# Optimization experiments

Hardware: AMD Instinct MI355X
Metric: run time of the kernel (lower is better)

The kernel has to match this reference:

```python
import jax, jax.numpy as jnp
import numpy as np

N = 10000      # nodes
E = 80000      # edges (avg degree 8)
G = 64         # graphs in batch
HID = 256
RBF_K = 16
DEPTH = 6
KA, KC, KE = 16, 6, 5
DE = HID // 3          # 85, per-modality embedding dim
CAT = 3 * HID + RBF_K  # 784, width of [h_i, h_j, rbf, e_emb]
CUTOFF = 10.0


def _gumbel_hard(probs, noise, tau=1.0):
    """F.gumbel_softmax(log(probs), tau, hard=True) with externally supplied gumbel noise."""
    logits = jnp.log(jnp.clip(probs, 1e-12))
    y = jax.nn.softmax((logits + noise) / tau, axis=-1)
    hard = jax.nn.one_hot(jnp.argmax(y, axis=-1), y.shape[-1], dtype=y.dtype)
    return hard + y - jax.lax.stop_gradient(y)  # straight-through


def setup_inputs() -> dict:
    key = jax.random.key(0)
    ks = iter(jax.random.split(key, 80))

    def nrm(shape, fan):
        return jax.random.normal(next(ks), shape, jnp.float32) / np.sqrt(fan).astype(np.float32)

    def gumbel(shape):
        u = jax.random.uniform(next(ks), shape, minval=1e-9, maxval=1.0 - 1e-9)
        return -jnp.log(-jnp.log(u))

    inp = {}
    inp['a_t'] = jax.random.uniform(next(ks), (N, KA))
    inp['c_t'] = jax.random.uniform(next(ks), (N, KC))
    inp['e_t'] = jax.random.uniform(next(ks), (E, KE))
    inp['x_t'] = jax.random.normal(next(ks), (N, 3))
    inp['g_a'] = gumbel((N, KA))
    inp['g_c'] = gumbel((N, KC))
    inp['g_e'] = gumbel((E, KE))

    # embeddings / fuse / lift
    inp['atom_W'] = nrm((KA, DE), KA)
    inp['charge_W'] = nrm((KC, DE), KC)
    inp['bond_W'] = nrm((KE, DE), KE)
    inp['fuse_W'] = nrm((3 * DE, HID), 3 * DE)
    inp['fuse_b'] = jnp.zeros((HID,))
    inp['lift_W'] = nrm((DE, HID), DE)
    inp['lift_b'] = jnp.zeros((HID,))

    # stacked block params (DEPTH blocks)
    inp['phim_W1'] = nrm((DEPTH, CAT, HID), CAT)
    inp['phim_b1'] = jnp.zeros((DEPTH, HID))
    inp['phim_W2'] = nrm((DEPTH, HID, HID), HID)
    inp['phim_b2'] = jnp.zeros((DEPTH, HID))
    inp['phix_W1'] = nrm((DEPTH, HID, HID), HID)
    inp['phix_b1'] = jnp.zeros((DEPTH, HID))
    inp['phix_W2'] = nrm((DEPTH, HID, 1), HID)
    inp['phix_b2'] = jnp.zeros((DEPTH, 1))
    inp['psim_W1'] = nrm((DEPTH, CAT, HID), CAT)
    inp['psim_b1'] = jnp.zeros((DEPTH, HID))
    inp['psim_W2'] = nrm((DEPTH, HID, HID), HID)
    inp['psim_b2'] = jnp.zeros((DEPTH, HID))
    inp['updh_W1'] = nrm((DEPTH, 2 * HID, HID), 2 * HID)
    inp['updh_b1'] = jnp.zeros((DEPTH, HID))
    inp['updh_W2'] = nrm((DEPTH, HID, HID), HID)
    inp['updh_b2'] = jnp.zeros((DEPTH, HID))
    inp['ln_g'] = jnp.ones((DEPTH, HID))
    inp['ln_b'] = jnp.zeros((DEPTH, HID))
    inp['head_W'] = nrm((HID, 1), HID)
    inp['head_b'] = jnp.zeros((1,))

    inp['src'] = jax.random.randint(next(ks), (E,), 0, N)
    inp['dst'] = jax.random.randint(next(ks), (E,), 0, N)
    inp['node_graph'] = jnp.sort(jax.random.randint(next(ks), (N,), 0, G))
    return inp


def reference(a_t, c_t, e_t, x_t, g_a, g_c, g_e,
              atom_W, charge_W, bond_W, fuse_W, fuse_b, lift_W, lift_b,
              phim_W1, phim_b1, phim_W2, phim_b2,
              phix_W1, phix_b1, phix_W2, phix_b2,
              psim_W1, psim_b1, psim_W2, psim_b2,
              updh_W1, updh_b1, updh_W2, updh_b2,
              ln_g, ln_b, head_W, head_b,
              src, dst, node_graph):
    centers = jnp.linspace(0.0, CUTOFF, RBF_K)
    widths = jnp.full((RBF_K,), CUTOFF / RBF_K)

    # encode nodes: gumbel-hard embed atom & charge probs, zero x-slot, fuse
    a_h = _gumbel_hard(a_t, g_a) @ atom_W           # (N, DE)
    c_h = _gumbel_hard(c_t, g_c) @ charge_W         # (N, DE)
    h = jnp.concatenate([a_h, c_h, jnp.zeros_like(a_h)], axis=-1) @ fuse_W + fuse_b  # (N, HID)
    # encode edges
    e_emb = (_gumbel_hard(e_t, g_e) @ bond_W) @ lift_W + lift_b  # (E, HID)

    x = x_t
    for d in range(DEPTH):
        h_i, h_j = h[dst], h[src]                    # gather per edge
        rij = x[dst] - x[src]                        # (E, 3)
        dist = jnp.sqrt(jnp.clip(jnp.sum(rij * rij, -1, keepdims=True), 0.0))
        z = (dist - centers) / (widths + 1e-12)
        rbf = jnp.exp(-0.5 * z * z)                  # (E, RBF_K)
        cat = jnp.concatenate([h_i, h_j, rbf, e_emb], axis=-1)  # (E, 784)
        m = jax.nn.silu(jax.nn.silu(cat @ phim_W1[d] + phim_b1[d]) @ phim_W2[d] + phim_b2[d])
        gate = jax.nn.silu(m @ phix_W1[d] + phix_b1[d]) @ phix_W2[d] + phix_b2[d]  # (E, 1)
        pm = jax.nn.silu(jax.nn.silu(cat @ psim_W1[d] + psim_b1[d]) @ psim_W2[d] + psim_b2[d])
        dx_sum = jax.ops.segment_sum(rij * gate, dst, num_segments=N)   # scatter to dst
        pm_sum = jax.ops.segment_sum(pm, dst, num_segments=N)
        x = x + dx_sum
        u = jax.nn.silu(jnp.concatenate([h, pm_sum], -1) @ updh_W1[d] + updh_b1[d]) @ updh_W2[d] + updh_b2[d]
        z2 = h + u
        mu = jnp.mean(z2, -1, keepdims=True)
        var = jnp.mean((z2 - mu) ** 2, -1, keepdims=True)
        h = (z2 - mu) / jnp.sqrt(var + 1e-5) * ln_g[d] + ln_b[d]

    # mean readout per graph
    cnt = jax.ops.segment_sum(jnp.ones((h.shape[0], 1), h.dtype), node_graph, num_segments=G)
    hg = jax.ops.segment_sum(h, node_graph, num_segments=G) / jnp.maximum(cnt, 1.0)
    out = jax.nn.sigmoid((hg @ head_W + head_b) / 2.0)  # property='score' -> sigmoid, tau=2
    return out
```

## Files before the change

kernel.cpp:

```cpp
#include <hip/hip_runtime.h>
#include <math.h>

#define NN   10000
#define NE   80000
#define NG   64
#define HID  256
#define RBFK 16
#define NDEP 6
#define KA   16
#define KC   6
#define KE   5
#define DE   85
#define CATW 784

typedef __attribute__((ext_vector_type(8))) short bf16x8;
typedef __attribute__((ext_vector_type(4))) float f32x4;
typedef __attribute__((ext_vector_type(2))) __bf16 bf16v2;

#if __has_builtin(__builtin_amdgcn_fdot2_f32_bf16)
#define HAVE_BF16_DOT2 1
#else
#define HAVE_BF16_DOT2 0
#endif

static __device__ __forceinline__ float silu_f(float v) {
  return __fdividef(v, 1.0f + __expf(-v));
}

static __device__ __forceinline__ unsigned short f2bf(float f) {
  union { float f; unsigned int u; } v; v.f = f;
  unsigned int r = v.u + 0x7fff + ((v.u >> 16) & 1);
  return (unsigned short)(r >> 16);
}
static __device__ __forceinline__ float bf2f(unsigned short h) {
  union { unsigned int u; float f; } v; v.u = ((unsigned int)h) << 16;
  return v.f;
}
static __device__ __forceinline__ bf16v2 u2bf2(unsigned int u) {
  union { unsigned int u; bf16v2 v; } x; x.u = u; return x.v;
}

static __device__ __forceinline__ void gload16(const void* g, void* l) {
  __builtin_amdgcn_global_load_lds((const __attribute__((address_space(1))) unsigned int*)g,
                                   (__attribute__((address_space(3))) unsigned int*)l, 16, 0, 0);
}

__global__ void convw_plain(const float* __restrict__ W, unsigned short* __restrict__ Wt, int K,
                            long long wt_dstride, int wt_rowoff) {
  __shared__ float T[32][65];
  int k0 = blockIdx.x * 32, n0 = blockIdx.y * 64, d = blockIdx.z;
  int tid = threadIdx.x;
  int nn = tid & 63, kr = tid >> 6;
  const float* Wd = W + (size_t)d * K * 256;
#pragma unroll
  for (int i = 0; i < 8; ++i) {
    int k = kr + i * 4;
    T[k][nn] = Wd[(size_t)(k0 + k) * 256 + n0 + nn];
  }
  __syncthreads();
  unsigned short* Wtd = Wt + (size_t)d * wt_dstride;
  int kk = tid & 31, nr = tid >> 5;
#pragma unroll
  for (int i = 0; i < 8; ++i) {
    int n = nr + i * 8;
    Wtd[(size_t)(wt_rowoff + n0 + n) * K + k0 + kk] = f2bf(T[kk][n]);
  }
}

__global__ void convw_nodeblk(const float* __restrict__ W, unsigned short* __restrict__ Wt,
                              int src_k0, int nt_base) {
  __shared__ float T[32][65];
  int k0 = blockIdx.x * 32, n0 = blockIdx.y * 64, d = blockIdx.z;
  int tid = threadIdx.x;
  int nn = tid & 63, kr = tid >> 6;
  const float* Wd = W + (size_t)d * CATW * 256;
#pragma unroll
  for (int i = 0; i < 8; ++i) {
    int k = kr + i * 4;
    T[k][nn] = Wd[(size_t)(src_k0 + k0 + k) * 256 + n0 + nn];
  }
  __syncthreads();
  unsigned short* Wtd = Wt + (size_t)d * 1024 * 256;
  int kk = tid & 31, nr = tid >> 5;
#pragma unroll
  for (int i = 0; i < 8; ++i) {
    int n = nr + i * 8;
    Wtd[(size_t)(nt_base + n0 + n) * 256 + k0 + kk] = f2bf(T[kk][n]);
  }
}

__global__ void convw_rbf(const float* __restrict__ phimW1, const float* __restrict__ psimW1,
                          unsigned short* __restrict__ wR) {
  int d = blockIdx.x, j = threadIdx.x;
  int jj = j & 255;
  const float* W = (j < 256) ? phimW1 : psimW1;
  for (int k = 0; k < 16; ++k)
    wR[((size_t)d * 16 + k) * 512 + j] = f2bf(W[(size_t)d * CATW * 256 + (size_t)(512 + k) * 256 + jj]);
}

__global__ void convw_rbf2(const float* __restrict__ phimW1, const float* __restrict__ psimW1,
                           unsigned int* __restrict__ wRp) {
  int d = blockIdx.x, j = threadIdx.x;
  int jj = j & 255;
  const float* W = (j < 256) ? phimW1 : psimW1;
  const float* base = W + (size_t)d * CATW * 256;
  for (int p = 0; p < 8; ++p) {
    unsigned int lo = f2bf(base[(size_t)(512 + 2*p) * 256 + jj]);
    unsigned int hi = f2bf(base[(size_t)(512 + 2*p + 1) * 256 + jj]);
    wRp[((size_t)d * 8 + p) * 512 + j] = lo | (hi << 16);
  }
}

__global__ void tables_kernel(const float* __restrict__ atom_W, const float* __restrict__ charge_W,
                              const float* __restrict__ bond_W, const float* __restrict__ fuse_W,
                              const float* __restrict__ fuse_b, const float* __restrict__ lift_W,
                              const float* __restrict__ lift_b,
                              float* __restrict__ tabA, float* __restrict__ tabC,
                              float* __restrict__ tabEf) {
  int r = blockIdx.x, k = threadIdx.x;
  if (r < KA) {
    float s = 0.f;
    for (int d = 0; d < DE; ++d) s += atom_W[r*DE + d] * fuse_W[d*HID + k];
    tabA[r*HID + k] = s + fuse_b[k];
  } else if (r < KA + KC) {
    int rr = r - KA;
    float s = 0.f;
    for (int d = 0; d < DE; ++d) s += charge_W[rr*DE + d] * fuse_W[(DE + d)*HID + k];
    tabC[rr*HID + k] = s;
  } else {
    int rr = r - KA - KC;
    float s = 0.f;
    for (int d = 0; d < DE; ++d) s += bond_W[rr*DE + d] * lift_W[d*HID + k];
    tabEf[rr*HID + k] = s + lift_b[k];
  }
}

__global__ void tabe1_kernel(const float* __restrict__ tabEf,
                             const float* __restrict__ phimW1, const float* __restrict__ phimb1,
                             const float* __restrict__ psimW1, const float* __restrict__ psimb1,
                             unsigned short* __restrict__ tabE1) {
  int r = blockIdx.x, d = blockIdx.y, j = threadIdx.x;
  const float* W = (j < 256) ? phimW1 : psimW1;
  const float* b = (j < 256) ? phimb1 : psimb1;
  int jj = j & 255;
  float s = b[d*256 + jj];
  for (int k = 0; k < 256; ++k)
    s += tabEf[r*256 + k] * W[(size_t)d*CATW*256 + (size_t)(528 + k)*256 + jj];
  tabE1[((size_t)d*5 + r)*512 + j] = f2bf(s);
}

__global__ void node_init_kernel(const float* __restrict__ a_t, const float* __restrict__ c_t,
                                 const float* __restrict__ g_a, const float* __restrict__ g_c,
                                 const float* __restrict__ x_t, const float* __restrict__ tabA,
                                 const float* __restrict__ tabC, float* __restrict__ h,
                                 unsigned short* __restrict__ hbf, float* __restrict__ x) {
  int n = blockIdx.x;
  __shared__ int s_ia, s_ic;
  if (threadIdx.x == 0) {
    float best = -1e30f; int bi = 0;
    for (int j = 0; j < KA; ++j) {
      float v = logf(fmaxf(a_t[n*KA + j], 1e-12f)) + g_a[n*KA + j];
      if (v > best) { best = v; bi = j; }
    }
    s_ia = bi;
  }
  if (threadIdx.x == 1) {
    float best = -1e30f; int bi = 0;
    for (int j = 0; j < KC; ++j) {
      float v = logf(fmaxf(c_t[n*KC + j], 1e-12f)) + g_c[n*KC + j];
      if (v > best) { best = v; bi = j; }
    }
    s_ic = bi;
  }
  __syncthreads();
  int k = threadIdx.x;
  float v = tabA[s_ia*HID + k] + tabC[s_ic*HID + k];
  h[n*HID + k] = v;
  hbf[n*HID + k] = f2bf(v);
  if (k < 3) x[n*3 + k] = x_t[n*3 + k];
}

__global__ void edge_init_kernel(const float* __restrict__ e_t, const float* __restrict__ g_e,
                                 int* __restrict__ ie) {
  int e = blockIdx.x * blockDim.x + threadIdx.x;
  if (e >= NE) return;
  float best = -1e30f; int bi = 0;
  for (int j = 0; j < KE; ++j) {
    float v = logf(fmaxf(e_t[e*KE + j], 1e-12f)) + g_e[e*KE + j];
    if (v > best) { best = v; bi = j; }
  }
  ie[e] = bi;
}

__global__ void hist_kernel(const int* __restrict__ dst, int* __restrict__ deg) {
  int e = blockIdx.x * 256 + threadIdx.x;
  if (e < NE) atomicAdd(&deg[dst[e]], 1);
}

__global__ void scan_kernel(const int* __restrict__ deg, int* __restrict__ rowstart,
                            int* __restrict__ cursor) {
  __shared__ int tmp[1024];
  int t = threadIdx.x;
  int base = t * 10;
  int local[10];
  int s = 0;
#pragma unroll
  for (int i = 0; i < 10; ++i) { local[i] = deg[base + i]; s += local[i]; }
  tmp[t] = s;
  __syncthreads();
  for (int off = 1; off < 1024; off <<= 1) {
    int v = (t >= off) ? tmp[t - off] : 0;
    __syncthreads();
    tmp[t] += v;
    __syncthreads();
  }
  int run = (t == 0) ? 0 : tmp[t - 1];
#pragma unroll
  for (int i = 0; i < 10; ++i) {
    rowstart[base + i] = run; cursor[base + i] = run; run += local[i];
  }
  if (t == 1023) rowstart[10240] = run;
}

__global__ void fill_kernel(const int* __restrict__ dst, int* __restrict__ cursor,
                            int* __restrict__ eids) {
  int e = blockIdx.x * 256 + threadIdx.x;
  if (e >= NE) return;
  int pos = atomicAdd(&cursor[dst[e]], 1);
  eids[pos] = e;
}

__global__ void sortrows_kernel(const int* __restrict__ rowstart, int* __restrict__ eids) {
  int n = blockIdx.x * 256 + threadIdx.x;
  if (n >= NN) return;
  int s = rowstart[n], e = rowstart[n + 1];
  for (int i = s + 1; i < e; ++i) {
    int v = eids[i]; int j = i - 1;
    while (j >= s && eids[j] > v) { eids[j + 1] = eids[j]; --j; }
    eids[j + 1] = v;
  }
}

__global__ void gbound_kernel(const int* __restrict__ ng, int* __restrict__ gstart) {
  int n = blockIdx.x * 256 + threadIdx.x;
  if (n >= NN) return;
  if (n == 0) {
    for (int g = 0; g <= ng[0]; ++g) gstart[g] = 0;
  } else {
    int a = ng[n-1], b = ng[n];
    for (int g = a + 1; g <= b; ++g) gstart[g] = n;
  }
  if (n == NN - 1) {
    for (int g = ng[n] + 1; g <= NG; ++g) gstart[g] = NN;
  }
}

__global__ __launch_bounds__(256) void combine2_kernel(
    const int* __restrict__ srcp, const int* __restrict__ dstp, const int* __restrict__ iep,
    const float* __restrict__ x,
    const unsigned short* __restrict__ P,
    const unsigned short* __restrict__ tabE1,
    const unsigned short* __restrict__ wR,
    const unsigned int* __restrict__ wRp,
    unsigned short* __restrict__ c1, unsigned short* __restrict__ ps1) {
  const int tid = threadIdx.x;
  const int lane = tid & 63;
  const int e = blockIdx.x * 4 + (tid >> 6);
  const int half = lane >> 5;
  const int c8 = (lane & 31) * 8;
  const int ds = dstp[e], sr = srcp[e], ib = iep[e];
  float r0 = x[ds*3+0] - x[sr*3+0];
  float r1 = x[ds*3+1] - x[sr*3+1];
  float r2 = x[ds*3+2] - x[sr*3+2];
  float dist = sqrtf(r0*r0 + r1*r1 + r2*r2);
  int klo = (int)(dist * 1.5f) - 3;
  klo = klo < 0 ? 0 : (klo > 8 ? 8 : klo);
  const unsigned short* Pb0 = P + (size_t)(half * 2) * NN * 256;
  const unsigned short* Pb1 = P + (size_t)(half * 2 + 1) * NN * 256;
  bf16x8 pa = *(const bf16x8*)&Pb0[(size_t)ds * 256 + c8];
  bf16x8 pb = *(const bf16x8*)&Pb1[(size_t)sr * 256 + c8];
  bf16x8 te = *(const bf16x8*)&tabE1[(size_t)ib * 512 + lane * 8];
  float zv[8];
#pragma unroll
  for (int j = 0; j < 8; ++j)
    zv[j] = bf2f((unsigned short)pa[j]) + bf2f((unsigned short)pb[j]) + bf2f((unsigned short)te[j]);
#if HAVE_BF16_DOT2
  int plo = klo >> 1;
  if (plo > 4) plo = 4;
#pragma unroll
  for (int pp = 0; pp < 4; ++pp) {
    int pr = plo + pp;
    float k0f = (float)(2 * pr);
    float z0 = (dist - 0.66666667f * k0f) * 1.6f;
    float z1 = (dist - 0.66666667f * (k0f + 1.0f)) * 1.6f;
    unsigned int rkp = (unsigned int)f2bf(__expf(-0.5f * z0 * z0)) |
                       ((unsigned int)f2bf(__expf(-0.5f * z1 * z1)) << 16);
    bf16v2 rv = u2bf2(rkp);
    const unsigned int* w8 = wRp + (size_t)pr * 512 + lane * 8;
    uint4 wa = *(const uint4*)w8;
    uint4 wb = *(const uint4*)(w8 + 4);
    zv[0] = __builtin_amdgcn_fdot2_f32_bf16(rv, u2bf2(wa.x), zv[0], false);
    zv[1] = __builtin_amdgcn_fdot2_f32_bf16(rv, u2bf2(wa.y), zv[1], false);
    zv[2] = __builtin_amdgcn_fdot2_f32_bf16(rv, u2bf2(wa.z), zv[2], false);
    zv[3] = __builtin_amdgcn_fdot2_f32_bf16(rv, u2bf2(wa.w), zv[3], false);
    zv[4] = __builtin_amdgcn_fdot2_f32_bf16(rv, u2bf2(wb.x), zv[4], false);
    zv[5] = __builtin_amdgcn_fdot2_f32_bf16(rv, u2bf2(wb.y), zv[5], false);
    zv[6] = __builtin_amdgcn_fdot2_f32_bf16(rv, u2bf2(wb.z), zv[6], false);
    zv[7] = __builtin_amdgcn_fdot2_f32_bf16(rv, u2bf2(wb.w), zv[7], false);
  }
#else
  (void)wRp;
#pragma unroll
  for (int kk = 0; kk < 8; ++kk) {
    int k = klo + kk;
    float z = (dist - 0.66666667f * (float)k) * 1.6f;
    float rk = __expf(-0.5f * z * z);
    bf16x8 wv = *(const bf16x8*)&wR[k * 512 + lane * 8];
#pragma unroll
    for (int j = 0; j < 8; ++j)
      zv[j] += rk * bf2f((unsigned short)wv[j]);
  }
#endif
  unsigned short ov[8];
#pragma unroll
  for (int j = 0; j < 8; ++j) ov[j] = f2bf(silu_f(zv[j]));
  unsigned short* outp = half ? ps1 : c1;
  *(uint4*)&outp[(size_t)e * 256 + c8] = *(uint4*)ov;
}

template<int MODE, bool SILU, bool GATE, bool LNOUT, bool SMALL>
__global__ __launch_bounds__(SMALL ? 256 : 512, 4) void mfma_gemm(
    const unsigned short* __restrict__ A, const unsigned short* __restrict__ A2,
    const unsigned short* __restrict__ Wt,
    const float* __restrict__ bias, const float* __restrict__ bias2,
    unsigned short* __restrict__ C, unsigned short* __restrict__ C2,
    int M, int Kp, int Msplit,
    const float* __restrict__ gw2, float* __restrict__ gout,
    float* __restrict__ hf, unsigned short* __restrict__ hb,
    const float* __restrict__ lng, const float* __restrict__ lnb) {
  constexpr int BM = SMALL ? 64 : 128;
  constexpr int BQ = SMALL ? 8 : 4;
  __shared__ unsigned short lds[SMALL ? 20480 : 24576];
  unsigned short* As = lds;
  unsigned short* Bs = lds + BM * 64;
  const int tid = threadIdx.x;
  const int bn = blockIdx.x * 256;
  const int bm = blockIdx.y * BM;
  const int lane = tid & 63;
  const int w = tid >> 6;
  const int wr = SMALL ? 0 : (w >> 2);
  const int wc = SMALL ? w : (w & 3);
  const int subrow = lane >> 3;
  const int kd = 8 * ((lane & 7) ^ subrow);

  const bool half2 = (MODE == 4) && (bm >= Msplit);
  const unsigned short* Wb = Wt + (half2 ? 256 * 256 : 0);

  unsigned int offB[BQ];
#pragma unroll
  for (int q = 0; q < BQ; ++q)
    offB[q] = (unsigned)(bn + w * (BQ * 8) + q * 8 + subrow) * (unsigned)Kp;

  unsigned int offA[2];
#pragma unroll
  for (int q = 0; q < 2; ++q) {
    int m = bm + w * 16 + q * 8 + subrow;
    int mc = (m < M) ? m : (M - 1);
    offA[q] = (unsigned)mc * 256u;
  }

  const int nt = Kp >> 6;
  f32x4 acc[4][4] = {};

  for (int t = 0; t < nt; ++t) {
    const int k0 = t << 6;
#pragma unroll
    for (int q = 0; q < 2; ++q) {
      const unsigned short* gp;
      if (MODE == 2) gp = (k0 < 256) ? (A + offA[q] + k0 + kd) : (A2 + offA[q] + (k0 - 256) + kd);
      else gp = A + offA[q] + k0 + kd;
      gload16(gp, (char*)As + w * 2048 + q * 1024);
    }
#pragma unroll
    for (int q = 0; q < BQ; ++q)
      gload16(Wb + offB[q] + k0 + kd, (char*)Bs + w * (BQ * 1024) + q * 1024);
    __syncthreads();
#pragma unroll
    for (int ks = 0; ks < 2; ++ks) {
      const int kb = (ks * 64 + ((lane >> 4) << 4)) ^ ((lane & 7) << 4);
      bf16x8 bfv[4];
#pragma unroll
      for (int j = 0; j < 4; ++j)
        bfv[j] = *(const bf16x8*)((const char*)Bs + (wc * 64 + j * 16 + (lane & 15)) * 128 + kb);
#pragma unroll
      for (int i = 0; i < 4; ++i) {
        bf16x8 af = *(const bf16x8*)((const char*)As + (wr * 64 + i * 16 + (lane & 15)) * 128 + kb);
#pragma unroll
        for (int j = 0; j < 4; ++j)
          acc[i][j] = __builtin_amdgcn_mfma_f32_16x16x32_bf16(af, bfv[j], acc[i][j], 0, 0, 0);
      }
    }
    __syncthreads();
  }

  if (GATE) {
    float bcol[4], wcol[4];
#pragma unroll
    for (int j = 0; j < 4; ++j) {
      int col = wc * 64 + j * 16 + (lane & 15);
      bcol[j] = bias[col];
      wcol[j] = gw2[col];
    }
    float* part = (float*)lds;
#pragma unroll
    for (int i = 0; i < 4; ++i) {
#pragma unroll
      for (int q = 0; q < 4; ++q) {
        float lsum = 0.f;
#pragma unroll
        for (int j = 0; j < 4; ++j)
          lsum += silu_f(acc[i][j][q] + bcol[j]) * wcol[j];
        lsum += __shfl_xor(lsum, 1, 64);
        lsum += __shfl_xor(lsum, 2, 64);
        lsum += __shfl_xor(lsum, 4, 64);
        lsum += __shfl_xor(lsum, 8, 64);
        if ((lane & 15) == 0) {
          int rl = wr * 64 + i * 16 + ((lane >> 4) << 2) + q;
          part[wc * BM + rl] = lsum;
        }
      }
    }
    __syncthreads();
    if (tid < BM)
      gout[bm + tid] = part[tid] + part[BM + tid] + part[2*BM + tid] + part[3*BM + tid];
    return;
  }

  if (LNOUT) {
    float bcol[4], lgc[4], lbc[4];
#pragma unroll
    for (int j = 0; j < 4; ++j) {
      int col = wc * 64 + j * 16 + (lane & 15);
      bcol[j] = bias[col]; lgc[j] = lng[col]; lbc[j] = lnb[col];
    }
    float* part = (float*)lds;
    float* stat = part + 4 * BM;
#pragma unroll
    for (int i = 0; i < 4; ++i)
#pragma unroll
      for (int q = 0; q < 4; ++q) {
        int rl = wr * 64 + i * 16 + ((lane >> 4) << 2) + q;
        int grow = bm + rl;
        float s = 0.f;
#pragma unroll
        for (int j = 0; j < 4; ++j) {
          int col = wc * 64 + j * 16 + (lane & 15);
          float hv = (grow < M) ? hf[(size_t)grow * 256 + col] : 0.f;
          float zz = acc[i][j][q] + bcol[j] + hv;
          acc[i][j][q] = zz;
          s += zz;
        }
        s += __shfl_xor(s, 1, 64); s += __shfl_xor(s, 2, 64);
        s += __shfl_xor(s, 4, 64); s += __shfl_xor(s, 8, 64);
        if ((lane & 15) == 0) part[wc * BM + rl] = s;
      }
    __syncthreads();
    if (tid < BM)
      stat[tid] = (part[tid] + part[BM + tid] + part[2*BM + tid] + part[3*BM + tid]) * (1.f / 256.f);
    __syncthreads();
#pragma unroll
    for (int i = 0; i < 4; ++i)
#pragma unroll
      for (int q = 0; q < 4; ++q) {
        int rl = wr * 64 + i * 16 + ((lane >> 4) << 2) + q;
        float mu = stat[rl];
        float s2 = 0.f;
#pragma unroll
        for (int j = 0; j < 4; ++j) { float d_ = acc[i][j][q] - mu; s2 += d_ * d_; }
        s2 += __shfl_xor(s2, 1, 64); s2 += __shfl_xor(s2, 2, 64);
        s2 += __shfl_xor(s2, 4, 64); s2 += __shfl_xor(s2, 8, 64);
        if ((lane & 15) == 0) part[wc * BM + rl] = s2;
      }
    __syncthreads();
    if (tid < BM)
      stat[BM + tid] = 1.f / sqrtf((part[tid] + part[BM + tid] + part[2*BM + tid] + part[3*BM + tid]) * (1.f / 256.f) + 1e-5f);
    __syncthreads();
#pragma unroll
    for (int i = 0; i < 4; ++i)
#pragma unroll
      for (int q = 0; q < 4; ++q) {
        int rl = wr * 64 + i * 16 + ((lane >> 4) << 2) + q;
        int grow = bm + rl;
        if (grow < M) {
          float mu = stat[rl], rs = stat[BM + rl];
#pragma unroll
          for (int j = 0; j < 4; ++j) {
            int col = wc * 64 + j * 16 + (lane & 15);
            float o = (acc[i][j][q] - mu) * rs * lgc[j] + lbc[j];
            hf[(size_t)grow * 256 + col] = o;
            hb[(size_t)grow * 256 + col] = f2bf(o);
          }
        }
      }
    return;
  }

  const float* biasw = bias;
  unsigned short* Cw = C;
  int rowoff = 0;
  if (MODE == 3) Cw = C + (size_t)(bn >> 8) * (size_t)M * 256;
  if (MODE == 4 && half2) { biasw = bias2; Cw = C2; rowoff = Msplit; }

  float bcol[4];
#pragma unroll
  for (int j = 0; j < 4; ++j) bcol[j] = biasw[wc * 64 + j * 16 + (lane & 15)];

  unsigned short* T = lds;
#pragma unroll
  for (int hh = 0; hh < 2; ++hh) {
    if ((wc >> 1) == hh) {
#pragma unroll
      for (int i = 0; i < 4; ++i)
#pragma unroll
        for (int j = 0; j < 4; ++j)
#pragma unroll
          for (int q = 0; q < 4; ++q) {
            int rl = wr * 64 + i * 16 + ((lane >> 4) << 2) + q;
            int cl = (wc & 1) * 64 + j * 16 + (lane & 15);
            float v = acc[i][j][q] + bcol[j];
            if (SILU) v = silu_f(v);
            T[rl * 136 + cl] = f2bf(v);
          }
    }
    __syncthreads();
#pragma unroll
    for (int it = 0; it < 4; ++it) {
      int row = it * (BM / 4) + (tid >> 4);
      int grow = bm + row;
      if (grow < M) {
        uint4 v = *(const uint4*)&T[row * 136 + (tid & 15) * 8];
        *(uint4*)&Cw[(size_t)(grow - rowoff) * 256 + hh * 128 + (tid & 15) * 8] = v;
      }
    }
    __syncthreads();
  }
}

__global__ void gather_pm_dx(const unsigned short* __restrict__ pm, const float* __restrict__ gate,
                             const float* __restrict__ xcur, const int* __restrict__ srcp,
                             const int* __restrict__ rowstart, const int* __restrict__ eids,
                             const float* __restrict__ gb2,
                             unsigned short* __restrict__ pmbf, float* __restrict__ xnxt) {
  int n = blockIdx.x, k = threadIdx.x;
  int s = rowstart[n], e1 = rowstart[n + 1];
  float acc = 0.f, dx = 0.f;
  float b2 = gb2[0];
  float xn = (k < 3) ? xcur[n*3 + k] : 0.f;
  for (int t = s; t < e1; ++t) {
    int e = eids[t];
    acc += bf2f(pm[(size_t)e*HID + k]);
    if (k < 3) dx += (xn - xcur[srcp[e]*3 + k]) * (gate[e] + b2);
  }
  pmbf[(size_t)n*HID + k] = f2bf(acc);
  if (k < 3) xnxt[n*3 + k] = xn + dx;
}

__global__ void readout_kernel(const float* __restrict__ h, const int* __restrict__ gstart,
                               const float* __restrict__ head_W, const float* __restrict__ head_b,
                               float* __restrict__ out) {
  int g = blockIdx.x, k = threadIdx.x;
  int s = gstart[g], e = gstart[g + 1];
  float acc = 0.f;
  for (int n = s; n < e; ++n) acc += h[(size_t)n * HID + k];
  float v = acc * head_W[k];
  __shared__ float red[4];
  int lane = k & 63, wv = k >> 6;
#pragma unroll
  for (int off = 32; off > 0; off >>= 1) v += __shfl_down(v, off, 64);
  if (lane == 0) red[wv] = v;
  __syncthreads();
  if (k == 0) {
    float dot = red[0] + red[1] + red[2] + red[3];
    float c = fmaxf((float)(e - s), 1.0f);
    float val = (dot / c + head_b[0]) * 0.5f;
    out[g] = __fdividef(1.0f, 1.0f + __expf(-val));
  }
}

extern "C" void kernel_launch(void* const* d_in, const int* in_sizes, int n_in,
                              void* d_out, int out_size, void* d_ws, size_t ws_size,
                              hipStream_t stream) {
  (void)in_sizes; (void)n_in; (void)out_size; (void)ws_size;
  const float* a_t      = (const float*)d_in[0];
  const float* c_t      = (const float*)d_in[1];
  const float* e_t      = (const float*)d_in[2];
  const float* x_t      = (const float*)d_in[3];
  const float* g_a      = (const float*)d_in[4];
  const float* g_c      = (const float*)d_in[5];
  const float* g_e      = (const float*)d_in[6];
  const float* atom_W   = (const float*)d_in[7];
  const float* charge_W = (const float*)d_in[8];
  const float* bond_W   = (const float*)d_in[9];
  const float* fuse_W   = (const float*)d_in[10];
  const float* fuse_b   = (const float*)d_in[11];
  const float* lift_W   = (const float*)d_in[12];
  const float* lift_b   = (const float*)d_in[13];
  const float* phim_W1  = (const float*)d_in[14];
  const float* phim_b1  = (const float*)d_in[15];
  const float* phim_W2  = (const float*)d_in[16];
  const float* phim_b2  = (const float*)d_in[17];
  const float* phix_W1  = (const float*)d_in[18];
  const float* phix_b1  = (const float*)d_in[19];
  const float* phix_W2  = (const float*)d_in[20];
  const float* phix_b2  = (const float*)d_in[21];
  const float* psim_W1  = (const float*)d_in[22];
  const float* psim_b1  = (const float*)d_in[23];
  const float* psim_W2  = (const float*)d_in[24];
  const float* psim_b2  = (const float*)d_in[25];
  const float* updh_W1  = (const float*)d_in[26];
  const float* updh_b1  = (const float*)d_in[27];
  const float* updh_W2  = (const float*)d_in[28];
  const float* updh_b2  = (const float*)d_in[29];
  const float* ln_g     = (const float*)d_in[30];
  const float* ln_b     = (const float*)d_in[31];
  const float* head_W   = (const float*)d_in[32];
  const float* head_b   = (const float*)d_in[33];
  const int*   src      = (const int*)d_in[34];
  const int*   dst      = (const int*)d_in[35];
  const int*   ngraph   = (const int*)d_in[36];
  float* out = (float*)d_out;

  char* p = (char*)d_ws;
  auto carve = [&](size_t bytes) -> char* {
    char* r = p; p += (bytes + 255) & ~(size_t)255; return r;
  };
  float*          h     = (float*)carve((size_t)NN*HID*4);
  unsigned short* hbf   = (unsigned short*)carve((size_t)NN*HID*2);
  float*          xposA = (float*)carve((size_t)NN*3*4);
  float*          xposB = (float*)carve((size_t)NN*3*4);
  int*            ie    = (int*)carve((size_t)NE*4);
  float*          tabA  = (float*)carve((size_t)KA*HID*4);
  float*          tabC  = (float*)carve((size_t)KC*HID*4);
  float*          tabEf = (float*)carve((size_t)KE*HID*4);
  float*          gate  = (float*)carve((size_t)NE*4);
  unsigned short* pmbf  = (unsigned short*)carve((size_t)NN*HID*2);
  float*          zbias = (float*)carve(256*4);
  unsigned short* buf01 = (unsigned short*)carve((size_t)2*NE*HID*2);
  unsigned short* bufM  = (unsigned short*)carve((size_t)NE*HID*2);
  unsigned short* bufPM = (unsigned short*)carve((size_t)NE*HID*2);
  unsigned short* P     = (unsigned short*)carve((size_t)4*NN*HID*2);
  int* deg      = (int*)carve(10240*4);
  int* cursor   = (int*)carve(10240*4);
  int* rowstart = (int*)carve(10241*4);
  int* eids     = (int*)carve((size_t)NE*4);
  int* gstart   = (int*)carve((NG+1)*4);
  unsigned short* wNode  = (unsigned short*)carve((size_t)NDEP*1024*256*2);
  unsigned short* wMPM   = (unsigned short*)carve((size_t)NDEP*512*256*2);
  unsigned short* wPhix1 = (unsigned short*)carve((size_t)NDEP*256*256*2);
  unsigned short* wUpd1  = (unsigned short*)carve((size_t)NDEP*256*512*2);
  unsigned short* wUpd2  = (unsigned short*)carve((size_t)NDEP*256*256*2);
  unsigned short* wRbf   = (unsigned short*)carve((size_t)NDEP*16*512*2);
  unsigned int*   wRbfP  = (unsigned int*)carve((size_t)NDEP*8*512*4);
  unsigned short* tabE1  = (unsigned short*)carve((size_t)NDEP*5*512*2);

  unsigned short* c1buf = buf01;
  unsigned short* psbuf = buf01 + (size_t)NE*HID;

  convw_nodeblk<<<dim3(8,4,NDEP), 256, 0, stream>>>(phim_W1, wNode, 0,   0);
  convw_nodeblk<<<dim3(8,4,NDEP), 256, 0, stream>>>(phim_W1, wNode, 256, 256);
  convw_nodeblk<<<dim3(8,4,NDEP), 256, 0, stream>>>(psim_W1, wNode, 0,   512);
  convw_nodeblk<<<dim3(8,4,NDEP), 256, 0, stream>>>(psim_W1, wNode, 256, 768);
  convw_plain<<<dim3(8,4,NDEP), 256, 0, stream>>>(phim_W2, wMPM, 256, 512*256, 0);
  convw_plain<<<dim3(8,4,NDEP), 256, 0, stream>>>(psim_W2, wMPM, 256, 512*256, 256);
  convw_plain<<<dim3(8,4,NDEP), 256, 0, stream>>>(phix_W1, wPhix1, 256, 256*256, 0);
  convw_plain<<<dim3(8,4,NDEP), 256, 0, stream>>>(updh_W2, wUpd2, 256, 256*256, 0);
  convw_plain<<<dim3(16,4,NDEP), 256, 0, stream>>>(updh_W1, wUpd1, 512, 256*512, 0);
  convw_rbf<<<NDEP, 512, 0, stream>>>(phim_W1, psim_W1, wRbf);
  convw_rbf2<<<NDEP, 512, 0, stream>>>(phim_W1, psim_W1, wRbfP);
  hipMemsetAsync(zbias, 0, 256*4, stream);

  tables_kernel<<<KA + KC + KE, 256, 0, stream>>>(atom_W, charge_W, bond_W, fuse_W, fuse_b,
                                                  lift_W, lift_b, tabA, tabC, tabEf);
  tabe1_kernel<<<dim3(5, NDEP), 512, 0, stream>>>(tabEf, phim_W1, phim_b1, psim_W1, psim_b1, tabE1);
  node_init_kernel<<<NN, 256, 0, stream>>>(a_t, c_t, g_a, g_c, x_t, tabA, tabC, h, hbf, xposA);
  edge_init_kernel<<<(NE + 255)/256, 256, 0, stream>>>(e_t, g_e, ie);

  hipMemsetAsync(deg, 0, 10240*4, stream);
  hist_kernel<<<(NE + 255)/256, 256, 0, stream>>>(dst, deg);
  scan_kernel<<<1, 1024, 0, stream>>>(deg, rowstart, cursor);
  fill_kernel<<<(NE + 255)/256, 256, 0, stream>>>(dst, cursor, eids);
  sortrows_kernel<<<(NN + 255)/256, 256, 0, stream>>>(rowstart, eids);
  gbound_kernel<<<(NN + 255)/256, 256, 0, stream>>>(ngraph, gstart);

  dim3 gridP(4, (NN + 63)/64);
  dim3 gridE(1, NE/128);
  dim3 gridE2(1, 2*NE/128);
  dim3 gridNS(1, (NN + 63)/64);

  float* xcur = xposA;
  float* xnxt = xposB;

  for (int d = 0; d < NDEP; ++d) {
    const float* pb2m = phim_b2 + (size_t)d*HID;
    const float* pxb1 = phix_b1 + (size_t)d*HID;
    const float* pxW2 = phix_W2 + (size_t)d*HID;
    const float* pxb2 = phix_b2 + (size_t)d;
    const float* psb2 = psim_b2 + (size_t)d*HID;
    const float* pub1 = updh_b1 + (size_t)d*HID;
    const float* pub2 = updh_b2 + (size_t)d*HID;

    mfma_gemm<3, false, false, false, true><<<gridP, 256, 0, stream>>>(
        hbf, nullptr, wNode + (size_t)d*1024*256, zbias, nullptr, P, nullptr, NN, 256, 0,
        nullptr, nullptr, nullptr, nullptr, nullptr, nullptr);
    combine2_kernel<<<NE/4, 256, 0, stream>>>(
        src, dst, ie, xcur, P, tabE1 + (size_t)d*5*512, wRbf + (size_t)d*16*512,
        wRbfP + (size_t)d*8*512, c1buf, psbuf);
    mfma_gemm<4, true, false, false, false><<<gridE2, 512, 0, stream>>>(
        buf01, nullptr, wMPM + (size_t)d*512*256, pb2m, psb2, bufM, bufPM, 2*NE, 256, NE,
        nullptr, nullptr, nullptr, nullptr, nullptr, nullptr);
    mfma_gemm<0, false, true, false, false><<<gridE, 512, 0, stream>>>(
        bufM, nullptr, wPhix1 + (size_t)d*256*256, pxb1, nullptr, nullptr, nullptr, NE, 256, 0,
        pxW2, gate, nullptr, nullptr, nullptr, nullptr);
    gather_pm_dx<<<NN, 256, 0, stream>>>(bufPM, gate, xcur, src, rowstart, eids, pxb2, pmbf, xnxt);
    mfma_gemm<2, true, false, false, true><<<gridNS, 256, 0, stream>>>(
        hbf, pmbf, wUpd1 + (size_t)d*256*512, pub1, nullptr, bufM, nullptr, NN, 512, 0,
        nullptr, nullptr, nullptr, nullptr, nullptr, nullptr);
    mfma_gemm<0, false, false, true, true><<<gridNS, 256, 0, stream>>>(
        bufM, nullptr, wUpd2 + (size_t)d*256*256, pub2, nullptr, nullptr, nullptr, NN, 256, 0,
        nullptr, nullptr, h, hbf, ln_g + (size_t)d*HID, ln_b + (size_t)d*HID);

    float* tmp = xcur; xcur = xnxt; xnxt = tmp;
  }

  readout_kernel<<<NG, 256, 0, stream>>>(h, gstart, head_W, head_b, out);
}
```

Baseline: 1.555 ms.

## Fuse node-update MLP layers and LayerNorm into a single kernel

Replaces the two node-update GEMM launches (concat[h,pm]→256 with SiLU, then 256→256 with residual and LayerNorm) with one kernel. Each block keeps its 64-row intermediate activation in LDS as bf16 and runs the second GEMM and LayerNorm straight from it. This removes the global round trip of the intermediate buffer and one launch per layer. In exchange the work is spread over fewer blocks (157 blocks of 64 rows), LDS use is larger, and there is no double buffering of weight loads.

```diff
diff --git a/kernel.cpp b/kernel.cpp
--- a/kernel.cpp
+++ b/kernel.cpp
@@ -543,6 +543,184 @@
       }
     }
     __syncthreads();
+  }
+}
+
+__global__ __launch_bounds__(256, 2) void upd_fused_kernel(
+    const unsigned short* __restrict__ hbf, const unsigned short* __restrict__ pmbf,
+    const unsigned short* __restrict__ W1t,
+    const unsigned short* __restrict__ W2t,
+    const float* __restrict__ b1, const float* __restrict__ b2,
+    float* __restrict__ hf, unsigned short* __restrict__ hb,
+    const float* __restrict__ lng, const float* __restrict__ lnb, int M) {
+  __shared__ unsigned short lds[16384 + 16896];
+  unsigned short* Bs = lds;
+  unsigned short* As = lds + 16384;
+  unsigned short* T  = lds + 16384;
+  const int tid = threadIdx.x;
+  const int bm = blockIdx.y * 64;
+  const int lane = tid & 63;
+  const int w = tid >> 6;
+  const int subrow = lane >> 3;
+  const int kd = 8 * ((lane & 7) ^ subrow);
+
+  unsigned int offA[2];
+#pragma unroll
+  for (int q = 0; q < 2; ++q) {
+    int m = bm + w * 16 + q * 8 + subrow;
+    int mc = (m < M) ? m : (M - 1);
+    offA[q] = (unsigned)mc * 256u;
+  }
+  unsigned int offB1[8];
+#pragma unroll
+  for (int q = 0; q < 8; ++q)
+    offB1[q] = (unsigned)(w * 64 + q * 8 + subrow) * 512u;
+
+  f32x4 acc[4][4] = {};
+  for (int t = 0; t < 8; ++t) {
+    const int k0 = t << 6;
+#pragma unroll
+    for (int q = 0; q < 2; ++q) {
+      const unsigned short* gp = (k0 < 256) ? (hbf + offA[q] + k0 + kd)
+                                            : (pmbf + offA[q] + (k0 - 256) + kd);
+      gload16(gp, (char*)As + w * 2048 + q * 1024);
+    }
+#pragma unroll
+    for (int q = 0; q < 8; ++q)
+      gload16(W1t + offB1[q] + k0 + kd, (char*)Bs + w * 8192 + q * 1024);
+    __syncthreads();
+#pragma unroll
+    for (int ks = 0; ks < 2; ++ks) {
+      const int kb = (ks * 64 + ((lane >> 4) << 4)) ^ ((lane & 7) << 4);
+      bf16x8 bfv[4];
+#pragma unroll
+      for (int j = 0; j < 4; ++j)
+        bfv[j] = *(const bf16x8*)((const char*)Bs + (w * 64 + j * 16 + (lane & 15)) * 128 + kb);
+#pragma unroll
+      for (int i = 0; i < 4; ++i) {
+        bf16x8 af = *(const bf16x8*)((const char*)As + (i * 16 + (lane & 15)) * 128 + kb);
+#pragma unroll
+        for (int j = 0; j < 4; ++j)
+          acc[i][j] = __builtin_amdgcn_mfma_f32_16x16x32_bf16(af, bfv[j], acc[i][j], 0, 0, 0);
+      }
+    }
+    __syncthreads();
+  }
+
+  {
+    float bcol[4];
+#pragma unroll
+    for (int j = 0; j < 4; ++j) bcol[j] = b1[w * 64 + j * 16 + (lane & 15)];
+#pragma unroll
+    for (int i = 0; i < 4; ++i)
+#pragma unroll
+      for (int j = 0; j < 4; ++j)
+#pragma unroll
+        for (int q = 0; q < 4; ++q) {
+          int rl = i * 16 + ((lane >> 4) << 2) + q;
+          int cl = w * 64 + j * 16 + (lane & 15);
+          T[rl * 264 + cl] = f2bf(silu_f(acc[i][j][q] + bcol[j]));
+        }
+  }
+  __syncthreads();
+
+  unsigned int offB2[8];
+#pragma unroll
+  for (int q = 0; q < 8; ++q)
+    offB2[q] = (unsigned)(w * 64 + q * 8 + subrow) * 256u;
+
+  f32x4 acc2[4][4] = {};
+  for (int t = 0; t < 4; ++t) {
+    const int k0 = t << 6;
+#pragma unroll
+    for (int q = 0; q < 8; ++q)
+      gload16(W2t + offB2[q] + k0 + kd, (char*)Bs + w * 8192 + q * 1024);
+    __syncthreads();
+#pragma unroll
+    for (int ks = 0; ks < 2; ++ks) {
+      const int kb = (ks * 64 + ((lane >> 4) << 4)) ^ ((lane & 7) << 4);
+      const int ka = k0 + ks * 32 + ((lane >> 4) << 3);
+      bf16x8 bfv[4];
+#pragma unroll
+      for (int j = 0; j < 4; ++j)
+        bfv[j] = *(const bf16x8*)((const char*)Bs + (w * 64 + j * 16 + (lane & 15)) * 128 + kb);
+#pragma unroll
+      for (int i = 0; i < 4; ++i) {
+        bf16x8 af = *(const bf16x8*)&T[(i * 16 + (lane & 15)) * 264 + ka];
+#pragma unroll
+        for (int j = 0; j < 4; ++j)
+          acc2[i][j] = __builtin_amdgcn_mfma_f32_16x16x32_bf16(af, bfv[j], acc2[i][j], 0, 0, 0);
+      }
+    }
+    __syncthreads();
+  }
+
+  {
+    float bcol[4], lgc[4], lbc[4];
+#pragma unroll
+    for (int j = 0; j < 4; ++j) {
+      int col = w * 64 + j * 16 + (lane & 15);
+      bcol[j] = b2[col]; lgc[j] = lng[col]; lbc[j] = lnb[col];
+    }
+    float* part = (float*)lds;
+    float* stat = part + 256;
+#pragma unroll
+    for (int i = 0; i < 4; ++i)
+#pragma unroll
+      for (int q = 0; q < 4; ++q) {
+        int rl = i * 16 + ((lane >> 4) << 2) + q;
+        int grow = bm + rl;
+        float s = 0.f;
+#pragma unroll
+        for (int j = 0; j < 4; ++j) {
+          int col = w * 64 + j * 16 + (lane & 15);
+          float hv = (grow < M) ? hf[(size_t)grow * 256 + col] : 0.f;
+          float zz = acc2[i][j][q] + bcol[j] + hv;
+          acc2[i][j][q] = zz;
+          s += zz;
+        }
+        s += __shfl_xor(s, 1, 64); s += __shfl_xor(s, 2, 64);
+        s += __shfl_xor(s, 4, 64); s += __shfl_xor(s, 8, 64);
+        if ((lane & 15) == 0) part[w * 64 + rl] = s;
+      }
+    __syncthreads();
+    if (tid < 64)
+      stat[tid] = (part[tid] + part[64 + tid] + part[128 + tid] + part[192 + tid]) * (1.f / 256.f);
+    __syncthreads();
+#pragma unroll
+    for (int i = 0; i < 4; ++i)
+#pragma unroll
+      for (int q = 0; q < 4; ++q) {
+        int rl = i * 16 + ((lane >> 4) << 2) + q;
+        float mu = stat[rl];
+        float s2 = 0.f;
+#pragma unroll
+        for (int j = 0; j < 4; ++j) { float d_ = acc2[i][j][q] - mu; s2 += d_ * d_; }
+        s2 += __shfl_xor(s2, 1, 64); s2 += __shfl_xor(s2, 2, 64);
+        s2 += __shfl_xor(s2, 4, 64); s2 += __shfl_xor(s2, 8, 64);
+        if ((lane & 15) == 0) part[w * 64 + rl] = s2;
+      }
+    __syncthreads();
+    if (tid < 64)
+      stat[64 + tid] = 1.f / sqrtf((part[tid] + part[64 + tid] + part[128 + tid] + part[192 + tid]) * (1.f / 256.f) + 1e-5f);
+    __syncthreads();
+#pragma unroll
+    for (int i = 0; i < 4; ++i)
+#pragma unroll
+      for (int q = 0; q < 4; ++q) {
+        int rl = i * 16 + ((lane >> 4) << 2) + q;
+        int grow = bm + rl;
+        if (grow < M) {
+          float mu = stat[rl], rs = stat[64 + rl];
+#pragma unroll
+          for (int j = 0; j < 4; ++j) {
+            int col = w * 64 + j * 16 + (lane & 15);
+            float o = (acc2[i][j][q] - mu) * rs * lgc[j] + lbc[j];
+            hf[(size_t)grow * 256 + col] = o;
+            hb[(size_t)grow * 256 + col] = f2bf(o);
+          }
+        }
+      }
   }
 }
 
@@ -695,7 +873,7 @@
   dim3 gridP(4, (NN + 63)/64);
   dim3 gridE(1, NE/128);
   dim3 gridE2(1, 2*NE/128);
-  dim3 gridNS(1, (NN + 63)/64);
+  dim3 gridNU(1, (NN + 63)/64);
 
   float* xcur = xposA;
   float* xnxt = xposB;
@@ -722,12 +900,9 @@
         bufM, nullptr, wPhix1 + (size_t)d*256*256, pxb1, nullptr, nullptr, nullptr, NE, 256, 0,
         pxW2, gate, nullptr, nullptr, nullptr, nullptr);
     gather_pm_dx<<<NN, 256, 0, stream>>>(bufPM, gate, xcur, src, rowstart, eids, pxb2, pmbf, xnxt);
-    mfma_gemm<2, true, false, false, true><<<gridNS, 256, 0, stream>>>(
-        hbf, pmbf, wUpd1 + (size_t)d*256*512, pub1, nullptr, bufM, nullptr, NN, 512, 0,
-        nullptr, nullptr, nullptr, nullptr, nullptr, nullptr);
-    mfma_gemm<0, false, false, true, true><<<gridNS, 256, 0, stream>>>(
-        bufM, nullptr, wUpd2 + (size_t)d*256*256, pub2, nullptr, nullptr, nullptr, NN, 256, 0,
-        nullptr, nullptr, h, hbf, ln_g + (size_t)d*HID, ln_b + (size_t)d*HID);
+    upd_fused_kernel<<<gridNU, 256, 0, stream>>>(
+        hbf, pmbf, wUpd1 + (size_t)d*256*512, wUpd2 + (size_t)d*256*256,
+        pub1, pub2, h, hbf, ln_g + (size_t)d*HID, ln_b + (size_t)d*HID, NN);
 
     float* tmp = xcur; xcur = xnxt; xnxt = tmp;
   }
```

Measured after the change: 1.374 ms. -11.7%, faster.
